# Optimization experiments

Measured on AMD Instinct MI355X. Metric: run time of the kernel, lower is better.

Reference implementation:

```python
import jax, jax.numpy as jnp
import numpy as np
import math

B, S, D, H, NC, K = 16, 512, 128, 8, 4, 7
DK = D // H
LN_EPS = 1e-5


def setup_inputs() -> dict:
    key = jax.random.key(0)
    ks = jax.random.split(key, 12)
    rn = lambda i, shape, scale: jax.random.normal(ks[i], shape, jnp.float32) * scale
    return {
        "x": rn(0, (B, S, D), 1.0),
        "mask": jnp.ones((B, S), jnp.int32),
        "ln_scale": jnp.ones((NC + 2, D), jnp.float32),
        "ln_bias": jnp.zeros((NC + 2, D), jnp.float32),
        "dw_w": rn(1, (NC, D, 1, K), 0.15),   # depthwise conv weights (OIH per layer)
        "dw_b": jnp.zeros((NC, D), jnp.float32),
        "pw_w": rn(2, (NC, D, D, 1), 0.08),   # pointwise conv weights
        "pw_b": jnp.zeros((NC, D), jnp.float32),
        "Wq": rn(3, (H, D, DK), 0.1),
        "Wk": rn(4, (H, D, DK), 0.1),
        "Wv": rn(5, (H, D, DK), 0.1),
        "Wo": rn(6, (D, D), 0.08),
        "att_bias": jnp.zeros((1,), jnp.float32),
        "f1_w": rn(7, (D, D), 0.08),
        "f1_b": jnp.zeros((D,), jnp.float32),
        "f2_w": rn(8, (D, D), 0.08),
        "f2_b": jnp.zeros((D,), jnp.float32),
        "l": 1,
        "blks": 7,
    }


def _ln(x, g, b):
    mu = jnp.mean(x, axis=-1, keepdims=True)
    var = jnp.mean((x - mu) ** 2, axis=-1, keepdims=True)
    return (x - mu) / jnp.sqrt(var + LN_EPS) * g + b


def _pos_signal(length, channels):
    position = jnp.arange(length, dtype=jnp.float32)
    nt = channels // 2
    inc = math.log(10000.0) / float(nt - 1)
    inv = jnp.exp(jnp.arange(nt, dtype=jnp.float32) * -inc)
    st = position[:, None] * inv[None, :]              # [L, nt]
    return jnp.concatenate([jnp.sin(st), jnp.cos(st)], axis=1)[None]  # [1, L, C]


def _encoder_block(x, mask, ln_scale, ln_bias, dw_w, dw_b, pw_w, pw_b,
                   Wq, Wk, Wv, Wo, att_bias, f1_w, f1_b, f2_w, f2_b):
    Bb, Ss, Dd = x.shape
    n_conv = dw_w.shape[0]
    k_size = dw_w.shape[-1]
    pad = k_size // 2
    dn = ('NCH', 'OIH', 'NCH')

    out = x + _pos_signal(Ss, Dd)
    # depthwise-separable conv stack (eval mode: dropout = identity)
    for i in range(n_conv):
        res = out
        h = _ln(out, ln_scale[i], ln_bias[i])
        hc = jnp.transpose(h, (0, 2, 1))  # [B, D, S]
        y = jax.lax.conv_general_dilated(hc, dw_w[i], (1,), [(pad, pad)],
                                         dimension_numbers=dn,
                                         feature_group_count=Dd)
        y = y + dw_b[i][None, :, None]
        y = jax.lax.conv_general_dilated(y, pw_w[i], (1,), [(0, 0)],
                                         dimension_numbers=dn)
        y = jax.nn.relu(y + pw_b[i][None, :, None])
        out = jnp.transpose(y, (0, 2, 1)) + res

    # multi-head self-attention (batched over heads, same math as per-head loop)
    res = out
    h = _ln(out, ln_scale[-2], ln_bias[-2])
    b0 = att_bias[0]
    q = jnp.einsum('bsd,hdk->bhsk', h, Wq) + b0
    k = jnp.einsum('bsd,hdk->bhsk', h, Wk) + b0
    v = jnp.einsum('bsd,hdk->bhsk', h, Wv) + b0
    scores = jnp.einsum('bhsk,bhtk->bhst', q, k) * (1.0 / math.sqrt(q.shape[-1]))
    m = mask.astype(scores.dtype)[:, None, None, :]  # mask over key axis
    scores = m * scores + (1.0 - m) * (-1e30)
    p = jax.nn.softmax(scores, axis=-1)
    att = jnp.einsum('bhst,bhtk->bhsk', p, v)          # [B,H,S,dk]
    mh = jnp.transpose(att, (0, 2, 1, 3)).reshape(Bb, Ss, Dd)
    out = mh @ Wo + b0 + res

    # feed-forward
    res = out
    h = _ln(out, ln_scale[-1], ln_bias[-1])
    h = jax.nn.relu(h @ f1_w.T + f1_b) @ f2_w.T + f2_b
    return h + res


def reference(x, mask, ln_scale, ln_bias, dw_w, dw_b, pw_w, pw_b,
              Wq, Wk, Wv, Wo, att_bias, f1_w, f1_b, f2_w, f2_b, l, blks):
    # l, blks only affect stochastic layer-dropout during training; eval = residual add
    return _encoder_block(x, mask, ln_scale, ln_bias, dw_w, dw_b, pw_w, pw_b,
                          Wq, Wk, Wv, Wo, att_bias, f1_w, f1_b, f2_w, f2_b)
```

## Files before the change

kernel.cpp:

```cpp
#include <hip/hip_runtime.h>
#include <math.h>

#define BB 16
#define SS 512
#define DD 128
#define HH 8
#define NCONV 4
#define KW 7
#define DKK 16
#define NN (BB*SS)
#define LN_EPS 1e-5f

typedef __attribute__((ext_vector_type(8))) short short8;
typedef __attribute__((ext_vector_type(4))) short short4v;
typedef __attribute__((ext_vector_type(4))) float f4;

static __device__ __forceinline__ ushort f2bf(float x) {
  union { float f; unsigned u; } v; v.f = x;
  unsigned r = v.u + 0x7fffu + ((v.u >> 16) & 1u);
  return (ushort)(r >> 16);
}

static __device__ __forceinline__ float posenc(int s, int col) {
  const float inc = 0.14619588f;
  int c = col & 63;
  float invf = expf(-inc * (float)c);
  float st = (float)s * invf;
  return (col < 64) ? sinf(st) : cosf(st);
}

__global__ __launch_bounds__(256) void prep_kernel(
    const float* __restrict__ pw, const float* __restrict__ Wq,
    const float* __restrict__ Wk, const float* __restrict__ Wv,
    const float* __restrict__ Wo, const float* __restrict__ f1,
    const float* __restrict__ f2, ushort* __restrict__ dst) {
  int i = blockIdx.x * 256 + threadIdx.x;
  if (i < 65536) { dst[i] = f2bf(pw[i]); return; }
  int j = i - 65536;
  if (j < 49152) {
    int o = j >> 7, d = j & 127;
    int sec = o >> 7, oo = o & 127, hh = oo >> 4, kk = oo & 15;
    const float* s = (sec == 0) ? Wq : ((sec == 1) ? Wk : Wv);
    dst[i] = f2bf(s[hh*2048 + d*16 + kk]); return;
  }
  j -= 49152;
  if (j < 16384) { int o = j >> 7, d = j & 127; dst[i] = f2bf(Wo[d*128 + o]); return; }
  j -= 16384;
  if (j < 16384) { dst[i] = f2bf(f1[j]); return; }
  j -= 16384;
  dst[i] = f2bf(f2[j]);
}

template<int LNORM, int ACT, int BIASMODE, int RES, int OUTBF>
__global__ __launch_bounds__(256) void mm16_kernel(
    const float* __restrict__ in_f, const ushort* __restrict__ in_b,
    const ushort* __restrict__ Wb,
    const float* __restrict__ gamma, const float* __restrict__ beta,
    const float* __restrict__ bias, const float* __restrict__ res,
    float* __restrict__ out_f, ushort* __restrict__ out_b, int ostride) {
  __shared__ ushort abuf[16*152];
  __shared__ ushort wbuf[128*152];
  int t = threadIdx.x;
  int r0 = blockIdx.x * 16;
  int ocol0 = blockIdx.y * 128;
  const ushort* W = Wb + blockIdx.y * (128*128);

  for (int i = t; i < 128*16; i += 256) {
    int row = i >> 4, ch = i & 15;
    *(short8*)&wbuf[row*152 + ch*8] = *(const short8*)&W[row*128 + ch*8];
  }
  int wv = t >> 6, lane = t & 63;
  if (LNORM) {
    for (int i = wv; i < 16; i += 4) {
      int r = r0 + i;
      float2 xv = *(const float2*)&in_f[r*128 + lane*2];
      float s1 = xv.x + xv.y, s2 = xv.x*xv.x + xv.y*xv.y;
      #pragma unroll
      for (int o = 32; o > 0; o >>= 1) { s1 += __shfl_xor(s1, o); s2 += __shfl_xor(s2, o); }
      float mu = s1 * (1.0f/128.0f);
      float var = s2 * (1.0f/128.0f) - mu*mu;
      float inv = rsqrtf(var + LN_EPS);
      float2 gv = *(const float2*)&gamma[lane*2];
      float2 bv = *(const float2*)&beta[lane*2];
      float n0 = (xv.x - mu)*inv*gv.x + bv.x;
      float n1 = (xv.y - mu)*inv*gv.y + bv.y;
      unsigned pk = (unsigned)f2bf(n0) | ((unsigned)f2bf(n1) << 16);
      *(unsigned*)&abuf[i*152 + lane*2] = pk;
    }
  } else {
    for (int i = t; i < 16*16; i += 256) {
      int row = i >> 4, ch = i & 15;
      *(short8*)&abuf[row*152 + ch*8] = *(const short8*)&in_b[(r0+row)*128 + ch*8];
    }
  }
  __syncthreads();

  int m = lane & 15, qd = lane >> 4;
  int c0 = wv * 32;
  f4 acc0 = {0.f,0.f,0.f,0.f}, acc1 = {0.f,0.f,0.f,0.f};
  #pragma unroll
  for (int ks = 0; ks < 4; ++ks) {
    short8 a  = *(const short8*)&abuf[m*152 + ks*32 + qd*8];
    short8 b0 = *(const short8*)&wbuf[(c0 + m)*152 + ks*32 + qd*8];
    short8 b1 = *(const short8*)&wbuf[(c0 + 16 + m)*152 + ks*32 + qd*8];
    acc0 = __builtin_amdgcn_mfma_f32_16x16x32_bf16(a, b0, acc0, 0, 0, 0);
    acc1 = __builtin_amdgcn_mfma_f32_16x16x32_bf16(a, b1, acc1, 0, 0, 0);
  }
  int col0 = c0 + m, col1 = c0 + 16 + m;
  float bv0 = (BIASMODE==1) ? bias[col0] : ((BIASMODE==2) ? bias[0] : 0.0f);
  float bv1 = (BIASMODE==1) ? bias[col1] : ((BIASMODE==2) ? bias[0] : 0.0f);
  #pragma unroll
  for (int reg = 0; reg < 4; ++reg) {
    int r = r0 + qd*4 + reg;
    float v0 = acc0[reg] + bv0, v1 = acc1[reg] + bv1;
    if (ACT) { v0 = fmaxf(v0, 0.0f); v1 = fmaxf(v1, 0.0f); }
    if (RES) { v0 += res[r*128 + col0]; v1 += res[r*128 + col1]; }
    if (OUTBF) {
      out_b[r*ostride + ocol0 + col0] = f2bf(v0);
      out_b[r*ostride + ocol0 + col1] = f2bf(v1);
    } else {
      out_f[r*ostride + ocol0 + col0] = v0;
      out_f[r*ostride + ocol0 + col1] = v1;
    }
  }
}

template<int ADDPOS>
__global__ __launch_bounds__(256) void conv_fused_kernel(
    const float* __restrict__ cur, const ushort* __restrict__ pwW,
    const float* __restrict__ gamma, const float* __restrict__ beta,
    const float* __restrict__ dww, const float* __restrict__ dwb,
    const float* __restrict__ pwb, float* __restrict__ out) {
  __shared__ float  hbuf[22*128];
  __shared__ ushort ybuf[16*152];
  __shared__ ushort wbuf[128*152];
  int t = threadIdx.x;
  int r0 = blockIdx.x * 16;
  int s0 = r0 & (SS-1);
  int bb = r0 >> 9;

  for (int i = t; i < 128*16; i += 256) {
    int row = i >> 4, ch = i & 15;
    *(short8*)&wbuf[row*152 + ch*8] = *(const short8*)&pwW[row*128 + ch*8];
  }
  int wv = t >> 6, lane = t & 63;
  for (int i = wv; i < 22; i += 4) {
    int s = s0 - 3 + i;
    if (s < 0 || s >= SS) {
      *(float2*)&hbuf[i*128 + lane*2] = make_float2(0.f, 0.f);
      continue;
    }
    int r = bb*SS + s;
    float2 xv = *(const float2*)&cur[r*128 + lane*2];
    if (ADDPOS) { xv.x += posenc(s, lane*2); xv.y += posenc(s, lane*2+1); }
    float s1 = xv.x + xv.y, s2 = xv.x*xv.x + xv.y*xv.y;
    #pragma unroll
    for (int o = 32; o > 0; o >>= 1) { s1 += __shfl_xor(s1, o); s2 += __shfl_xor(s2, o); }
    float mu = s1 * (1.0f/128.0f);
    float var = s2 * (1.0f/128.0f) - mu*mu;
    float inv = rsqrtf(var + LN_EPS);
    float2 gv = *(const float2*)&gamma[lane*2];
    float2 bv = *(const float2*)&beta[lane*2];
    hbuf[i*128 + lane*2]     = (xv.x - mu)*inv*gv.x + bv.x;
    hbuf[i*128 + lane*2 + 1] = (xv.y - mu)*inv*gv.y + bv.y;
  }
  __syncthreads();

  {
    int col = t & 127, rg = t >> 7;
    float w0 = dww[col*7+0], w1 = dww[col*7+1], w2 = dww[col*7+2], w3 = dww[col*7+3];
    float w4 = dww[col*7+4], w5 = dww[col*7+5], w6 = dww[col*7+6];
    float bs = dwb[col];
    #pragma unroll
    for (int rr = rg*8; rr < rg*8 + 8; ++rr) {
      float acc = bs;
      acc += hbuf[(rr+0)*128 + col] * w0;
      acc += hbuf[(rr+1)*128 + col] * w1;
      acc += hbuf[(rr+2)*128 + col] * w2;
      acc += hbuf[(rr+3)*128 + col] * w3;
      acc += hbuf[(rr+4)*128 + col] * w4;
      acc += hbuf[(rr+5)*128 + col] * w5;
      acc += hbuf[(rr+6)*128 + col] * w6;
      ybuf[rr*152 + col] = f2bf(acc);
    }
  }
  __syncthreads();

  int m = lane & 15, qd = lane >> 4;
  int c0 = wv * 32;
  f4 acc0 = {0.f,0.f,0.f,0.f}, acc1 = {0.f,0.f,0.f,0.f};
  #pragma unroll
  for (int ks = 0; ks < 4; ++ks) {
    short8 a  = *(const short8*)&ybuf[m*152 + ks*32 + qd*8];
    short8 b0 = *(const short8*)&wbuf[(c0 + m)*152 + ks*32 + qd*8];
    short8 b1 = *(const short8*)&wbuf[(c0 + 16 + m)*152 + ks*32 + qd*8];
    acc0 = __builtin_amdgcn_mfma_f32_16x16x32_bf16(a, b0, acc0, 0, 0, 0);
    acc1 = __builtin_amdgcn_mfma_f32_16x16x32_bf16(a, b1, acc1, 0, 0, 0);
  }
  int col0 = c0 + m, col1 = c0 + 16 + m;
  float bv0 = pwb[col0], bv1 = pwb[col1];
  #pragma unroll
  for (int reg = 0; reg < 4; ++reg) {
    int r = r0 + qd*4 + reg;
    int s = s0 + qd*4 + reg;
    float v0 = fmaxf(acc0[reg] + bv0, 0.0f);
    float v1 = fmaxf(acc1[reg] + bv1, 0.0f);
    float rz0 = cur[r*128 + col0], rz1 = cur[r*128 + col1];
    if (ADDPOS) { rz0 += posenc(s, col0); rz1 += posenc(s, col1); }
    out[r*128 + col0] = v0 + rz0;
    out[r*128 + col1] = v1 + rz1;
  }
}

__global__ __launch_bounds__(256) void attn_mfma_kernel(
    const ushort* __restrict__ qkv, const int* __restrict__ mask,
    ushort* __restrict__ att) {
  __shared__ ushort kbuf[512*24];
  __shared__ ushort vbuf[512*20];
  __shared__ ushort pbuf[4*16*40];
  __shared__ float  smask[512];
  int t = threadIdx.x;
  int blk = blockIdx.x;
  int qc = blk & 7, h = (blk >> 3) & 7, b = blk >> 6;

  for (int i = t; i < 512; i += 256) smask[i] = (float)mask[b*SS + i];
  for (int i = t; i < 1024; i += 256) {
    int s = i >> 1, half = i & 1;
    *(short8*)&kbuf[s*24 + half*8] =
      *(const short8*)&qkv[(size_t)(b*SS + s)*384 + 128 + h*16 + half*8];
  }
  for (int i = t; i < 2048; i += 256) {
    int s = i >> 2, qu = i & 3;
    *(short4v*)&vbuf[s*20 + qu*4] =
      *(const short4v*)&qkv[(size_t)(b*SS + s)*384 + 256 + h*16 + qu*4];
  }
  __syncthreads();

  int wv = t >> 6, lane = t & 63;
  int m = lane & 15, qd = lane >> 4;
  int qr0 = qc*64 + wv*16;

  short8 aq = (short8)0;
  if (qd < 2) aq = *(const short8*)&qkv[(size_t)(b*SS + qr0 + m)*384 + h*16 + qd*8];

  f4 oacc = {0.f,0.f,0.f,0.f};
  float lp0 = 0.f, lp1 = 0.f, lp2 = 0.f, lp3 = 0.f;
  ushort* pb = &pbuf[wv*640];
  f4 zz = {0.f,0.f,0.f,0.f};

  for (int step = 0; step < 16; ++step) {
    int kb = step * 32;
    short8 bk0 = (short8)0, bk1 = (short8)0;
    if (qd < 2) {
      bk0 = *(const short8*)&kbuf[(kb + m)*24 + qd*8];
      bk1 = *(const short8*)&kbuf[(kb + 16 + m)*24 + qd*8];
    }
    f4 s0 = __builtin_amdgcn_mfma_f32_16x16x32_bf16(aq, bk0, zz, 0, 0, 0);
    f4 s1 = __builtin_amdgcn_mfma_f32_16x16x32_bf16(aq, bk1, zz, 0, 0, 0);
    float mk0 = smask[kb + m], mk1 = smask[kb + 16 + m];
    #pragma unroll
    for (int reg = 0; reg < 4; ++reg) {
      float e0 = __expf(s0[reg] * 0.25f) * mk0;
      float e1 = __expf(s1[reg] * 0.25f) * mk1;
      if (reg == 0) { lp0 += e0 + e1; } else if (reg == 1) { lp1 += e0 + e1; }
      else if (reg == 2) { lp2 += e0 + e1; } else { lp3 += e0 + e1; }
      pb[(qd*4 + reg)*40 + m]      = f2bf(e0);
      pb[(qd*4 + reg)*40 + 16 + m] = f2bf(e1);
    }
    __asm__ volatile("s_waitcnt lgkmcnt(0)" ::: "memory");
    short8 ap = *(const short8*)&pb[m*40 + qd*8];
    short8 bv;
    #pragma unroll
    for (int j = 0; j < 8; ++j) bv[j] = (short)vbuf[(kb + qd*8 + j)*20 + m];
    oacc = __builtin_amdgcn_mfma_f32_16x16x32_bf16(ap, bv, oacc, 0, 0, 0);
  }

  float lp[4] = {lp0, lp1, lp2, lp3};
  #pragma unroll
  for (int reg = 0; reg < 4; ++reg) {
    float l = lp[reg];
    l += __shfl_xor(l, 1); l += __shfl_xor(l, 2);
    l += __shfl_xor(l, 4); l += __shfl_xor(l, 8);
    float ov = oacc[reg] / l;
    att[(size_t)(b*SS + qr0 + qd*4 + reg)*128 + h*16 + m] = f2bf(ov);
  }
}

extern "C" void kernel_launch(void* const* d_in, const int* in_sizes, int n_in,
                              void* d_out, int out_size, void* d_ws, size_t ws_size,
                              hipStream_t stream) {
  const float* x        = (const float*)d_in[0];
  const int*   mask     = (const int*)d_in[1];
  const float* ln_scale = (const float*)d_in[2];
  const float* ln_bias  = (const float*)d_in[3];
  const float* dw_w     = (const float*)d_in[4];
  const float* dw_b     = (const float*)d_in[5];
  const float* pw_w     = (const float*)d_in[6];
  const float* pw_b     = (const float*)d_in[7];
  const float* Wq       = (const float*)d_in[8];
  const float* Wk       = (const float*)d_in[9];
  const float* Wv       = (const float*)d_in[10];
  const float* Wo       = (const float*)d_in[11];
  const float* att_bias = (const float*)d_in[12];
  const float* f1_w     = (const float*)d_in[13];
  const float* f1_b     = (const float*)d_in[14];
  const float* f2_w     = (const float*)d_in[15];
  const float* f2_b     = (const float*)d_in[16];
  float* out = (float*)d_out;

  ushort* wall    = (ushort*)d_ws;
  ushort* pw_bf   = wall;
  ushort* wqkv_bf = wall + 65536;
  ushort* wo_bf   = wall + 114688;
  ushort* f1_bf   = wall + 131072;
  ushort* f2_bf   = wall + 147456;
  ushort* qkvbuf  = wall + 163840;
  ushort* attbuf  = qkvbuf + (size_t)NN*384;
  ushort* ybuf    = attbuf + (size_t)NN*128;

  hipLaunchKernelGGL(prep_kernel, dim3(640), dim3(256), 0, stream,
                     pw_w, Wq, Wk, Wv, Wo, f1_w, f2_w, wall);

  hipLaunchKernelGGL((conv_fused_kernel<1>), dim3(NN/16), dim3(256), 0, stream,
                     x, pw_bf, ln_scale, ln_bias, dw_w, dw_b, pw_b, out);
  for (int i = 1; i < NCONV; ++i) {
    hipLaunchKernelGGL((conv_fused_kernel<0>), dim3(NN/16), dim3(256), 0, stream,
                       out, pw_bf + i*16384, ln_scale + i*128, ln_bias + i*128,
                       dw_w + i*896, dw_b + i*128, pw_b + i*128, out);
  }

  hipLaunchKernelGGL((mm16_kernel<1,0,2,0,1>), dim3(NN/16, 3), dim3(256), 0, stream,
                     out, nullptr, wqkv_bf, ln_scale + 4*128, ln_bias + 4*128,
                     att_bias, nullptr, nullptr, qkvbuf, 384);

  hipLaunchKernelGGL(attn_mfma_kernel, dim3(BB*HH*8), dim3(256), 0, stream,
                     qkvbuf, mask, attbuf);

  hipLaunchKernelGGL((mm16_kernel<0,0,2,1,0>), dim3(NN/16, 1), dim3(256), 0, stream,
                     nullptr, attbuf, wo_bf, nullptr, nullptr,
                     att_bias, out, out, nullptr, 128);

  hipLaunchKernelGGL((mm16_kernel<1,1,1,0,1>), dim3(NN/16, 1), dim3(256), 0, stream,
                     out, nullptr, f1_bf, ln_scale + 5*128, ln_bias + 5*128,
                     f1_b, nullptr, nullptr, ybuf, 128);
  hipLaunchKernelGGL((mm16_kernel<0,0,1,1,0>), dim3(NN/16, 1), dim3(256), 0, stream,
                     nullptr, ybuf, f2_bf, nullptr, nullptr,
                     f2_b, out, out, nullptr, 128);
}
```

Before: 176.2 us.

## Fuse all stages into one cooperative persistent kernel with grid syncs

Replaces the ten separate kernel launches (weight prep, four conv layers, QKV, attention, Wo, FFN1, FFN2) with a single cooperative kernel of 512 blocks that runs each stage in turn, separated by grid.sync(). The tail fuses the Wo projection, layernorm, and both FFN matmuls per 16-row tile in shared memory. The conv layers ping-pong between two buffers, the depthwise conv is vectorised to float2, and V is stored transposed for the attention matmul. This removes launch gaps and intermediate global round-trips, at the cost of grid-barrier overhead and a fixed 512-block grid that may limit occupancy per stage.

```diff
diff --git a/kernel.cpp b/kernel.cpp
--- a/kernel.cpp
+++ b/kernel.cpp
@@ -1,13 +1,13 @@
 #include <hip/hip_runtime.h>
+#include <hip/hip_cooperative_groups.h>
 #include <math.h>
+
+namespace cg = cooperative_groups;
 
 #define BB 16
 #define SS 512
 #define DD 128
 #define HH 8
-#define NCONV 4
-#define KW 7
-#define DKK 16
 #define NN (BB*SS)
 #define LN_EPS 1e-5f
 
@@ -29,75 +29,15 @@
   return (col < 64) ? sinf(st) : cosf(st);
 }
 
-__global__ __launch_bounds__(256) void prep_kernel(
-    const float* __restrict__ pw, const float* __restrict__ Wq,
-    const float* __restrict__ Wk, const float* __restrict__ Wv,
-    const float* __restrict__ Wo, const float* __restrict__ f1,
-    const float* __restrict__ f2, ushort* __restrict__ dst) {
-  int i = blockIdx.x * 256 + threadIdx.x;
-  if (i < 65536) { dst[i] = f2bf(pw[i]); return; }
-  int j = i - 65536;
-  if (j < 49152) {
-    int o = j >> 7, d = j & 127;
-    int sec = o >> 7, oo = o & 127, hh = oo >> 4, kk = oo & 15;
-    const float* s = (sec == 0) ? Wq : ((sec == 1) ? Wk : Wv);
-    dst[i] = f2bf(s[hh*2048 + d*16 + kk]); return;
-  }
-  j -= 49152;
-  if (j < 16384) { int o = j >> 7, d = j & 127; dst[i] = f2bf(Wo[d*128 + o]); return; }
-  j -= 16384;
-  if (j < 16384) { dst[i] = f2bf(f1[j]); return; }
-  j -= 16384;
-  dst[i] = f2bf(f2[j]);
-}
-
-template<int LNORM, int ACT, int BIASMODE, int RES, int OUTBF>
-__global__ __launch_bounds__(256) void mm16_kernel(
-    const float* __restrict__ in_f, const ushort* __restrict__ in_b,
-    const ushort* __restrict__ Wb,
-    const float* __restrict__ gamma, const float* __restrict__ beta,
-    const float* __restrict__ bias, const float* __restrict__ res,
-    float* __restrict__ out_f, ushort* __restrict__ out_b, int ostride) {
-  __shared__ ushort abuf[16*152];
-  __shared__ ushort wbuf[128*152];
-  int t = threadIdx.x;
-  int r0 = blockIdx.x * 16;
-  int ocol0 = blockIdx.y * 128;
-  const ushort* W = Wb + blockIdx.y * (128*128);
-
-  for (int i = t; i < 128*16; i += 256) {
+static __device__ __forceinline__ void stage_w(ushort* wbuf, const ushort* W, int t) {
+  for (int i = t; i < 2048; i += 256) {
     int row = i >> 4, ch = i & 15;
     *(short8*)&wbuf[row*152 + ch*8] = *(const short8*)&W[row*128 + ch*8];
   }
-  int wv = t >> 6, lane = t & 63;
-  if (LNORM) {
-    for (int i = wv; i < 16; i += 4) {
-      int r = r0 + i;
-      float2 xv = *(const float2*)&in_f[r*128 + lane*2];
-      float s1 = xv.x + xv.y, s2 = xv.x*xv.x + xv.y*xv.y;
-      #pragma unroll
-      for (int o = 32; o > 0; o >>= 1) { s1 += __shfl_xor(s1, o); s2 += __shfl_xor(s2, o); }
-      float mu = s1 * (1.0f/128.0f);
-      float var = s2 * (1.0f/128.0f) - mu*mu;
-      float inv = rsqrtf(var + LN_EPS);
-      float2 gv = *(const float2*)&gamma[lane*2];
-      float2 bv = *(const float2*)&beta[lane*2];
-      float n0 = (xv.x - mu)*inv*gv.x + bv.x;
-      float n1 = (xv.y - mu)*inv*gv.y + bv.y;
-      unsigned pk = (unsigned)f2bf(n0) | ((unsigned)f2bf(n1) << 16);
-      *(unsigned*)&abuf[i*152 + lane*2] = pk;
-    }
-  } else {
-    for (int i = t; i < 16*16; i += 256) {
-      int row = i >> 4, ch = i & 15;
-      *(short8*)&abuf[row*152 + ch*8] = *(const short8*)&in_b[(r0+row)*128 + ch*8];
-    }
-  }
-  __syncthreads();
-
-  int m = lane & 15, qd = lane >> 4;
-  int c0 = wv * 32;
-  f4 acc0 = {0.f,0.f,0.f,0.f}, acc1 = {0.f,0.f,0.f,0.f};
+}
+
+static __device__ __forceinline__ void mm_tile(const ushort* abuf, const ushort* wbuf,
+                                               int m, int qd, int c0, f4& acc0, f4& acc1) {
   #pragma unroll
   for (int ks = 0; ks < 4; ++ks) {
     short8 a  = *(const short8*)&abuf[m*152 + ks*32 + qd*8];
@@ -106,43 +46,50 @@
     acc0 = __builtin_amdgcn_mfma_f32_16x16x32_bf16(a, b0, acc0, 0, 0, 0);
     acc1 = __builtin_amdgcn_mfma_f32_16x16x32_bf16(a, b1, acc1, 0, 0, 0);
   }
-  int col0 = c0 + m, col1 = c0 + 16 + m;
-  float bv0 = (BIASMODE==1) ? bias[col0] : ((BIASMODE==2) ? bias[0] : 0.0f);
-  float bv1 = (BIASMODE==1) ? bias[col1] : ((BIASMODE==2) ? bias[0] : 0.0f);
-  #pragma unroll
-  for (int reg = 0; reg < 4; ++reg) {
-    int r = r0 + qd*4 + reg;
-    float v0 = acc0[reg] + bv0, v1 = acc1[reg] + bv1;
-    if (ACT) { v0 = fmaxf(v0, 0.0f); v1 = fmaxf(v1, 0.0f); }
-    if (RES) { v0 += res[r*128 + col0]; v1 += res[r*128 + col1]; }
-    if (OUTBF) {
-      out_b[r*ostride + ocol0 + col0] = f2bf(v0);
-      out_b[r*ostride + ocol0 + col1] = f2bf(v1);
-    } else {
-      out_f[r*ostride + ocol0 + col0] = v0;
-      out_f[r*ostride + ocol0 + col1] = v1;
-    }
-  }
-}
-
-template<int ADDPOS>
-__global__ __launch_bounds__(256) void conv_fused_kernel(
-    const float* __restrict__ cur, const ushort* __restrict__ pwW,
-    const float* __restrict__ gamma, const float* __restrict__ beta,
-    const float* __restrict__ dww, const float* __restrict__ dwb,
-    const float* __restrict__ pwb, float* __restrict__ out) {
-  __shared__ float  hbuf[22*128];
-  __shared__ ushort ybuf[16*152];
-  __shared__ ushort wbuf[128*152];
+}
+
+static __device__ __forceinline__ void ln_rows_to_abuf(const float* in, int r0,
+    const float* gamma, const float* beta, ushort* abuf, int wv, int lane) {
+  for (int i = wv; i < 16; i += 4) {
+    float2 xv = *(const float2*)&in[(size_t)(r0 + i)*128 + lane*2];
+    float s1 = xv.x + xv.y, s2 = xv.x*xv.x + xv.y*xv.y;
+    #pragma unroll
+    for (int o = 32; o > 0; o >>= 1) { s1 += __shfl_xor(s1, o); s2 += __shfl_xor(s2, o); }
+    float mu  = s1 * (1.0f/128.0f);
+    float var = s2 * (1.0f/128.0f) - mu*mu;
+    float inv = rsqrtf(var + LN_EPS);
+    float2 gv = *(const float2*)&gamma[lane*2];
+    float2 bv = *(const float2*)&beta[lane*2];
+    float n0 = (xv.x - mu)*inv*gv.x + bv.x;
+    float n1 = (xv.y - mu)*inv*gv.y + bv.y;
+    unsigned pk = (unsigned)f2bf(n0) | ((unsigned)f2bf(n1) << 16);
+    *(unsigned*)&abuf[i*152 + lane*2] = pk;
+  }
+}
+
+struct MegaParams {
+  const float* x; const int* mask;
+  const float* ln_scale; const float* ln_bias;
+  const float* dw_w; const float* dw_b; const float* pw_w; const float* pw_b;
+  const float* Wq; const float* Wk; const float* Wv; const float* Wo;
+  const float* att_bias; const float* f1_w; const float* f1_b;
+  const float* f2_w; const float* f2_b;
+  float* out;
+  ushort* wbf; float* bufA; float* bufB; ushort* qkvbuf; ushort* attbuf;
+};
+
+static __device__ void conv_stage(unsigned char* smem, const float* in,
+    const ushort* pwW, const float* gamma, const float* beta,
+    const float* dww, const float* dwb, const float* pwb,
+    float* outp, bool addpos) {
+  float*  hbuf = (float*)smem;
+  ushort* wbuf = (ushort*)(smem + 11264);
+  ushort* ybuf = (ushort*)(smem + 50176);
   int t = threadIdx.x;
   int r0 = blockIdx.x * 16;
   int s0 = r0 & (SS-1);
   int bb = r0 >> 9;
-
-  for (int i = t; i < 128*16; i += 256) {
-    int row = i >> 4, ch = i & 15;
-    *(short8*)&wbuf[row*152 + ch*8] = *(const short8*)&pwW[row*128 + ch*8];
-  }
+  stage_w(wbuf, pwW, t);
   int wv = t >> 6, lane = t & 63;
   for (int i = wv; i < 22; i += 4) {
     int s = s0 - 3 + i;
@@ -151,12 +98,12 @@
       continue;
     }
     int r = bb*SS + s;
-    float2 xv = *(const float2*)&cur[r*128 + lane*2];
-    if (ADDPOS) { xv.x += posenc(s, lane*2); xv.y += posenc(s, lane*2+1); }
+    float2 xv = *(const float2*)&in[(size_t)r*128 + lane*2];
+    if (addpos) { xv.x += posenc(s, lane*2); xv.y += posenc(s, lane*2+1); }
     float s1 = xv.x + xv.y, s2 = xv.x*xv.x + xv.y*xv.y;
     #pragma unroll
     for (int o = 32; o > 0; o >>= 1) { s1 += __shfl_xor(s1, o); s2 += __shfl_xor(s2, o); }
-    float mu = s1 * (1.0f/128.0f);
+    float mu  = s1 * (1.0f/128.0f);
     float var = s2 * (1.0f/128.0f) - mu*mu;
     float inv = rsqrtf(var + LN_EPS);
     float2 gv = *(const float2*)&gamma[lane*2];
@@ -165,38 +112,30 @@
     hbuf[i*128 + lane*2 + 1] = (xv.y - mu)*inv*gv.y + bv.y;
   }
   __syncthreads();
-
   {
-    int col = t & 127, rg = t >> 7;
-    float w0 = dww[col*7+0], w1 = dww[col*7+1], w2 = dww[col*7+2], w3 = dww[col*7+3];
-    float w4 = dww[col*7+4], w5 = dww[col*7+5], w6 = dww[col*7+6];
-    float bs = dwb[col];
-    #pragma unroll
-    for (int rr = rg*8; rr < rg*8 + 8; ++rr) {
-      float acc = bs;
-      acc += hbuf[(rr+0)*128 + col] * w0;
-      acc += hbuf[(rr+1)*128 + col] * w1;
-      acc += hbuf[(rr+2)*128 + col] * w2;
-      acc += hbuf[(rr+3)*128 + col] * w3;
-      acc += hbuf[(rr+4)*128 + col] * w4;
-      acc += hbuf[(rr+5)*128 + col] * w5;
-      acc += hbuf[(rr+6)*128 + col] * w6;
-      ybuf[rr*152 + col] = f2bf(acc);
-    }
-  }
-  __syncthreads();
-
-  int m = lane & 15, qd = lane >> 4;
-  int c0 = wv * 32;
+    int cp = t & 63, rg = t >> 6;
+    float wa[7], wb2[7];
+    #pragma unroll
+    for (int k = 0; k < 7; ++k) { wa[k] = dww[(cp*2)*7 + k]; wb2[k] = dww[(cp*2+1)*7 + k]; }
+    float ba = dwb[cp*2], bbx = dwb[cp*2+1];
+    #pragma unroll
+    for (int j = 0; j < 4; ++j) {
+      int rr = rg*4 + j;
+      float a0 = ba, a1 = bbx;
+      #pragma unroll
+      for (int k = 0; k < 7; ++k) {
+        float2 hv = *(const float2*)&hbuf[(rr + k)*128 + cp*2];
+        a0 += hv.x * wa[k];
+        a1 += hv.y * wb2[k];
+      }
+      unsigned pk = (unsigned)f2bf(a0) | ((unsigned)f2bf(a1) << 16);
+      *(unsigned*)&ybuf[rr*152 + cp*2] = pk;
+    }
+  }
+  __syncthreads();
+  int m = lane & 15, qd = lane >> 4, c0 = wv*32;
   f4 acc0 = {0.f,0.f,0.f,0.f}, acc1 = {0.f,0.f,0.f,0.f};
-  #pragma unroll
-  for (int ks = 0; ks < 4; ++ks) {
-    short8 a  = *(const short8*)&ybuf[m*152 + ks*32 + qd*8];
-    short8 b0 = *(const short8*)&wbuf[(c0 + m)*152 + ks*32 + qd*8];
-    short8 b1 = *(const short8*)&wbuf[(c0 + 16 + m)*152 + ks*32 + qd*8];
-    acc0 = __builtin_amdgcn_mfma_f32_16x16x32_bf16(a, b0, acc0, 0, 0, 0);
-    acc1 = __builtin_amdgcn_mfma_f32_16x16x32_bf16(a, b1, acc1, 0, 0, 0);
-  }
+  mm_tile(ybuf, wbuf, m, qd, c0, acc0, acc1);
   int col0 = c0 + m, col1 = c0 + 16 + m;
   float bv0 = pwb[col0], bv1 = pwb[col1];
   #pragma unroll
@@ -205,25 +144,47 @@
     int s = s0 + qd*4 + reg;
     float v0 = fmaxf(acc0[reg] + bv0, 0.0f);
     float v1 = fmaxf(acc1[reg] + bv1, 0.0f);
-    float rz0 = cur[r*128 + col0], rz1 = cur[r*128 + col1];
-    if (ADDPOS) { rz0 += posenc(s, col0); rz1 += posenc(s, col1); }
-    out[r*128 + col0] = v0 + rz0;
-    out[r*128 + col1] = v1 + rz1;
-  }
-}
-
-__global__ __launch_bounds__(256) void attn_mfma_kernel(
-    const ushort* __restrict__ qkv, const int* __restrict__ mask,
-    ushort* __restrict__ att) {
-  __shared__ ushort kbuf[512*24];
-  __shared__ ushort vbuf[512*20];
-  __shared__ ushort pbuf[4*16*40];
-  __shared__ float  smask[512];
-  int t = threadIdx.x;
-  int blk = blockIdx.x;
-  int qc = blk & 7, h = (blk >> 3) & 7, b = blk >> 6;
-
-  for (int i = t; i < 512; i += 256) smask[i] = (float)mask[b*SS + i];
+    float rz0 = in[(size_t)r*128 + col0], rz1 = in[(size_t)r*128 + col1];
+    if (addpos) { rz0 += posenc(s, col0); rz1 += posenc(s, col1); }
+    outp[(size_t)r*128 + col0] = v0 + rz0;
+    outp[(size_t)r*128 + col1] = v1 + rz1;
+  }
+}
+
+static __device__ void qkv_stage(unsigned char* smem, const float* in,
+    const ushort* wqkv, const float* gamma, const float* beta,
+    float b0, ushort* qkvout) {
+  ushort* abuf = (ushort*)smem;
+  ushort* wbuf = (ushort*)(smem + 4864);
+  int t = threadIdx.x, wv = t >> 6, lane = t & 63;
+  int r0 = blockIdx.x * 16;
+  ln_rows_to_abuf(in, r0, gamma, beta, abuf, wv, lane);
+  int m = lane & 15, qd = lane >> 4, c0 = wv*32;
+  for (int c = 0; c < 3; ++c) {
+    __syncthreads();
+    stage_w(wbuf, wqkv + c*16384, t);
+    __syncthreads();
+    f4 acc0 = {0.f,0.f,0.f,0.f}, acc1 = {0.f,0.f,0.f,0.f};
+    mm_tile(abuf, wbuf, m, qd, c0, acc0, acc1);
+    int col0 = c0 + m, col1 = c0 + 16 + m;
+    #pragma unroll
+    for (int reg = 0; reg < 4; ++reg) {
+      int r = r0 + qd*4 + reg;
+      qkvout[(size_t)r*384 + c*128 + col0] = f2bf(acc0[reg] + b0);
+      qkvout[(size_t)r*384 + c*128 + col1] = f2bf(acc1[reg] + b0);
+    }
+  }
+}
+
+static __device__ void attn_stage(unsigned char* smem, const ushort* qkv,
+    const int* maskp, ushort* att) {
+  ushort* kbuf  = (ushort*)smem;
+  ushort* vT    = (ushort*)(smem + 24576);
+  ushort* pbuf  = (ushort*)(smem + 41216);
+  float*  smask = (float*)(smem + 46336);
+  int t = threadIdx.x, blk = blockIdx.x;
+  int qc = blk & 3, h = (blk >> 2) & 7, b = blk >> 5;
+  for (int i = t; i < 512; i += 256) smask[i] = (float)maskp[b*SS + i];
   for (int i = t; i < 1024; i += 256) {
     int s = i >> 1, half = i & 1;
     *(short8*)&kbuf[s*24 + half*8] =
@@ -231,119 +192,191 @@
   }
   for (int i = t; i < 2048; i += 256) {
     int s = i >> 2, qu = i & 3;
-    *(short4v*)&vbuf[s*20 + qu*4] =
-      *(const short4v*)&qkv[(size_t)(b*SS + s)*384 + 256 + h*16 + qu*4];
-  }
-  __syncthreads();
-
-  int wv = t >> 6, lane = t & 63;
-  int m = lane & 15, qd = lane >> 4;
-  int qr0 = qc*64 + wv*16;
-
-  short8 aq = (short8)0;
-  if (qd < 2) aq = *(const short8*)&qkv[(size_t)(b*SS + qr0 + m)*384 + h*16 + qd*8];
-
-  f4 oacc = {0.f,0.f,0.f,0.f};
-  float lp0 = 0.f, lp1 = 0.f, lp2 = 0.f, lp3 = 0.f;
+    short4v v = *(const short4v*)&qkv[(size_t)(b*SS + s)*384 + 256 + h*16 + qu*4];
+    #pragma unroll
+    for (int j = 0; j < 4; ++j) vT[(qu*4 + j)*520 + s] = (ushort)v[j];
+  }
+  __syncthreads();
+  int wv = t >> 6, lane = t & 63, m = lane & 15, qd = lane >> 4;
   ushort* pb = &pbuf[wv*640];
   f4 zz = {0.f,0.f,0.f,0.f};
-
-  for (int step = 0; step < 16; ++step) {
-    int kb = step * 32;
-    short8 bk0 = (short8)0, bk1 = (short8)0;
-    if (qd < 2) {
-      bk0 = *(const short8*)&kbuf[(kb + m)*24 + qd*8];
-      bk1 = *(const short8*)&kbuf[(kb + 16 + m)*24 + qd*8];
-    }
-    f4 s0 = __builtin_amdgcn_mfma_f32_16x16x32_bf16(aq, bk0, zz, 0, 0, 0);
-    f4 s1 = __builtin_amdgcn_mfma_f32_16x16x32_bf16(aq, bk1, zz, 0, 0, 0);
-    float mk0 = smask[kb + m], mk1 = smask[kb + 16 + m];
-    #pragma unroll
-    for (int reg = 0; reg < 4; ++reg) {
-      float e0 = __expf(s0[reg] * 0.25f) * mk0;
-      float e1 = __expf(s1[reg] * 0.25f) * mk1;
-      if (reg == 0) { lp0 += e0 + e1; } else if (reg == 1) { lp1 += e0 + e1; }
-      else if (reg == 2) { lp2 += e0 + e1; } else { lp3 += e0 + e1; }
-      pb[(qd*4 + reg)*40 + m]      = f2bf(e0);
-      pb[(qd*4 + reg)*40 + 16 + m] = f2bf(e1);
-    }
-    __asm__ volatile("s_waitcnt lgkmcnt(0)" ::: "memory");
-    short8 ap = *(const short8*)&pb[m*40 + qd*8];
-    short8 bv;
-    #pragma unroll
-    for (int j = 0; j < 8; ++j) bv[j] = (short)vbuf[(kb + qd*8 + j)*20 + m];
-    oacc = __builtin_amdgcn_mfma_f32_16x16x32_bf16(ap, bv, oacc, 0, 0, 0);
-  }
-
-  float lp[4] = {lp0, lp1, lp2, lp3};
-  #pragma unroll
-  for (int reg = 0; reg < 4; ++reg) {
-    float l = lp[reg];
-    l += __shfl_xor(l, 1); l += __shfl_xor(l, 2);
-    l += __shfl_xor(l, 4); l += __shfl_xor(l, 8);
-    float ov = oacc[reg] / l;
-    att[(size_t)(b*SS + qr0 + qd*4 + reg)*128 + h*16 + m] = f2bf(ov);
-  }
+  for (int sub = 0; sub < 2; ++sub) {
+    int qr0 = qc*128 + sub*64 + wv*16;
+    short8 aq = (short8)0;
+    if (qd < 2) aq = *(const short8*)&qkv[(size_t)(b*SS + qr0 + m)*384 + h*16 + qd*8];
+    f4 oacc = zz;
+    float lp0 = 0.f, lp1 = 0.f, lp2 = 0.f, lp3 = 0.f;
+    for (int step = 0; step < 16; ++step) {
+      int kb = step * 32;
+      short8 bk0 = (short8)0, bk1 = (short8)0;
+      if (qd < 2) {
+        bk0 = *(const short8*)&kbuf[(kb + m)*24 + qd*8];
+        bk1 = *(const short8*)&kbuf[(kb + 16 + m)*24 + qd*8];
+      }
+      f4 s0 = __builtin_amdgcn_mfma_f32_16x16x32_bf16(aq, bk0, zz, 0, 0, 0);
+      f4 s1 = __builtin_amdgcn_mfma_f32_16x16x32_bf16(aq, bk1, zz, 0, 0, 0);
+      float mk0 = smask[kb + m], mk1 = smask[kb + 16 + m];
+      #pragma unroll
+      for (int reg = 0; reg < 4; ++reg) {
+        float e0 = __expf(s0[reg] * 0.25f) * mk0;
+        float e1 = __expf(s1[reg] * 0.25f) * mk1;
+        if (reg == 0) lp0 += e0 + e1; else if (reg == 1) lp1 += e0 + e1;
+        else if (reg == 2) lp2 += e0 + e1; else lp3 += e0 + e1;
+        pb[(qd*4 + reg)*40 + m]      = f2bf(e0);
+        pb[(qd*4 + reg)*40 + 16 + m] = f2bf(e1);
+      }
+      __asm__ volatile("s_waitcnt lgkmcnt(0)" ::: "memory");
+      short8 ap = *(const short8*)&pb[m*40 + qd*8];
+      short8 bv = *(const short8*)&vT[m*520 + kb + qd*8];
+      oacc = __builtin_amdgcn_mfma_f32_16x16x32_bf16(ap, bv, oacc, 0, 0, 0);
+    }
+    float lp[4] = {lp0, lp1, lp2, lp3};
+    #pragma unroll
+    for (int reg = 0; reg < 4; ++reg) {
+      float l = lp[reg];
+      l += __shfl_xor(l, 1); l += __shfl_xor(l, 2);
+      l += __shfl_xor(l, 4); l += __shfl_xor(l, 8);
+      att[(size_t)(b*SS + qr0 + qd*4 + reg)*128 + h*16 + m] = f2bf(oacc[reg] / l);
+    }
+  }
+}
+
+static __device__ void tail_stage(unsigned char* smem, const ushort* attb,
+    const float* resA, const ushort* wo, const ushort* f1w, const ushort* f2w,
+    const float* gamma, const float* beta, float b0,
+    const float* f1_bias, const float* f2_bias, float* outp) {
+  float*  hres = (float*)smem;
+  ushort* wbuf = (ushort*)(smem + 8192);
+  ushort* abuf = (ushort*)(smem + 47104);
+  ushort* ybuf = (ushort*)(smem + 51968);
+  int t = threadIdx.x, wv = t >> 6, lane = t & 63;
+  int m = lane & 15, qd = lane >> 4, c0 = wv*32;
+  int r0 = blockIdx.x * 16;
+  stage_w(wbuf, wo, t);
+  for (int i = t; i < 256; i += 256) {
+    int row = i >> 4, ch = i & 15;
+    *(short8*)&abuf[row*152 + ch*8] = *(const short8*)&attb[(size_t)(r0 + row)*128 + ch*8];
+  }
+  __syncthreads();
+  {
+    f4 acc0 = {0.f,0.f,0.f,0.f}, acc1 = {0.f,0.f,0.f,0.f};
+    mm_tile(abuf, wbuf, m, qd, c0, acc0, acc1);
+    int col0 = c0 + m, col1 = c0 + 16 + m;
+    #pragma unroll
+    for (int reg = 0; reg < 4; ++reg) {
+      int lr = qd*4 + reg, r = r0 + lr;
+      hres[lr*128 + col0] = acc0[reg] + b0 + resA[(size_t)r*128 + col0];
+      hres[lr*128 + col1] = acc1[reg] + b0 + resA[(size_t)r*128 + col1];
+    }
+  }
+  __syncthreads();
+  ln_rows_to_abuf(hres, 0, gamma, beta, abuf, wv, lane);
+  stage_w(wbuf, f1w, t);
+  __syncthreads();
+  {
+    f4 acc0 = {0.f,0.f,0.f,0.f}, acc1 = {0.f,0.f,0.f,0.f};
+    mm_tile(abuf, wbuf, m, qd, c0, acc0, acc1);
+    int col0 = c0 + m, col1 = c0 + 16 + m;
+    float bv0 = f1_bias[col0], bv1 = f1_bias[col1];
+    #pragma unroll
+    for (int reg = 0; reg < 4; ++reg) {
+      int lr = qd*4 + reg;
+      ybuf[lr*152 + col0] = f2bf(fmaxf(acc0[reg] + bv0, 0.0f));
+      ybuf[lr*152 + col1] = f2bf(fmaxf(acc1[reg] + bv1, 0.0f));
+    }
+  }
+  __syncthreads();
+  stage_w(wbuf, f2w, t);
+  __syncthreads();
+  {
+    f4 acc0 = {0.f,0.f,0.f,0.f}, acc1 = {0.f,0.f,0.f,0.f};
+    mm_tile(ybuf, wbuf, m, qd, c0, acc0, acc1);
+    int col0 = c0 + m, col1 = c0 + 16 + m;
+    float bv0 = f2_bias[col0], bv1 = f2_bias[col1];
+    #pragma unroll
+    for (int reg = 0; reg < 4; ++reg) {
+      int lr = qd*4 + reg, r = r0 + lr;
+      outp[(size_t)r*128 + col0] = acc0[reg] + bv0 + hres[lr*128 + col0];
+      outp[(size_t)r*128 + col1] = acc1[reg] + bv1 + hres[lr*128 + col1];
+    }
+  }
+}
+
+__global__ __launch_bounds__(256, 2) void mega_kernel(MegaParams p) {
+  __shared__ __align__(16) unsigned char smem[57344];
+  cg::grid_group grid = cg::this_grid();
+  int t = threadIdx.x;
+
+  for (int i = blockIdx.x*256 + t; i < 163840; i += 131072) {
+    ushort val;
+    if (i < 65536) { val = f2bf(p.pw_w[i]); }
+    else {
+      int j = i - 65536;
+      if (j < 49152) {
+        int o = j >> 7, d = j & 127;
+        int sec = o >> 7, oo = o & 127, hh = oo >> 4, kk = oo & 15;
+        const float* s = (sec == 0) ? p.Wq : ((sec == 1) ? p.Wk : p.Wv);
+        val = f2bf(s[hh*2048 + d*16 + kk]);
+      } else {
+        j -= 49152;
+        if (j < 16384) { int o = j >> 7, d = j & 127; val = f2bf(p.Wo[d*128 + o]); }
+        else { j -= 16384;
+          if (j < 16384) val = f2bf(p.f1_w[j]);
+          else val = f2bf(p.f2_w[j - 16384]);
+        }
+      }
+    }
+    p.wbf[i] = val;
+  }
+  grid.sync();
+
+  conv_stage(smem, p.x,    p.wbf,         p.ln_scale,     p.ln_bias,     p.dw_w,       p.dw_b,       p.pw_b,       p.bufB, true);
+  grid.sync();
+  conv_stage(smem, p.bufB, p.wbf+16384, p.ln_scale+128, p.ln_bias+128, p.dw_w+896,  p.dw_b+128,  p.pw_b+128,  p.bufA, false);
+  grid.sync();
+  conv_stage(smem, p.bufA, p.wbf+32768, p.ln_scale+256, p.ln_bias+256, p.dw_w+1792, p.dw_b+256,  p.pw_b+256,  p.bufB, false);
+  grid.sync();
+  conv_stage(smem, p.bufB, p.wbf+49152, p.ln_scale+384, p.ln_bias+384, p.dw_w+2688, p.dw_b+384,  p.pw_b+384,  p.bufA, false);
+  grid.sync();
+
+  float b0 = p.att_bias[0];
+  qkv_stage(smem, p.bufA, p.wbf+65536, p.ln_scale+512, p.ln_bias+512, b0, p.qkvbuf);
+  grid.sync();
+  attn_stage(smem, p.qkvbuf, p.mask, p.attbuf);
+  grid.sync();
+  tail_stage(smem, p.attbuf, p.bufA, p.wbf+114688, p.wbf+131072, p.wbf+147456,
+             p.ln_scale+640, p.ln_bias+640, b0, p.f1_b, p.f2_b, p.out);
 }
 
 extern "C" void kernel_launch(void* const* d_in, const int* in_sizes, int n_in,
                               void* d_out, int out_size, void* d_ws, size_t ws_size,
                               hipStream_t stream) {
-  const float* x        = (const float*)d_in[0];
-  const int*   mask     = (const int*)d_in[1];
-  const float* ln_scale = (const float*)d_in[2];
-  const float* ln_bias  = (const float*)d_in[3];
-  const float* dw_w     = (const float*)d_in[4];
-  const float* dw_b     = (const float*)d_in[5];
-  const float* pw_w     = (const float*)d_in[6];
-  const float* pw_b     = (const float*)d_in[7];
-  const float* Wq       = (const float*)d_in[8];
-  const float* Wk       = (const float*)d_in[9];
-  const float* Wv       = (const float*)d_in[10];
-  const float* Wo       = (const float*)d_in[11];
-  const float* att_bias = (const float*)d_in[12];
-  const float* f1_w     = (const float*)d_in[13];
-  const float* f1_b     = (const float*)d_in[14];
-  const float* f2_w     = (const float*)d_in[15];
-  const float* f2_b     = (const float*)d_in[16];
-  float* out = (float*)d_out;
-
-  ushort* wall    = (ushort*)d_ws;
-  ushort* pw_bf   = wall;
-  ushort* wqkv_bf = wall + 65536;
-  ushort* wo_bf   = wall + 114688;
-  ushort* f1_bf   = wall + 131072;
-  ushort* f2_bf   = wall + 147456;
-  ushort* qkvbuf  = wall + 163840;
-  ushort* attbuf  = qkvbuf + (size_t)NN*384;
-  ushort* ybuf    = attbuf + (size_t)NN*128;
-
-  hipLaunchKernelGGL(prep_kernel, dim3(640), dim3(256), 0, stream,
-                     pw_w, Wq, Wk, Wv, Wo, f1_w, f2_w, wall);
-
-  hipLaunchKernelGGL((conv_fused_kernel<1>), dim3(NN/16), dim3(256), 0, stream,
-                     x, pw_bf, ln_scale, ln_bias, dw_w, dw_b, pw_b, out);
-  for (int i = 1; i < NCONV; ++i) {
-    hipLaunchKernelGGL((conv_fused_kernel<0>), dim3(NN/16), dim3(256), 0, stream,
-                       out, pw_bf + i*16384, ln_scale + i*128, ln_bias + i*128,
-                       dw_w + i*896, dw_b + i*128, pw_b + i*128, out);
-  }
-
-  hipLaunchKernelGGL((mm16_kernel<1,0,2,0,1>), dim3(NN/16, 3), dim3(256), 0, stream,
-                     out, nullptr, wqkv_bf, ln_scale + 4*128, ln_bias + 4*128,
-                     att_bias, nullptr, nullptr, qkvbuf, 384);
-
-  hipLaunchKernelGGL(attn_mfma_kernel, dim3(BB*HH*8), dim3(256), 0, stream,
-                     qkvbuf, mask, attbuf);
-
-  hipLaunchKernelGGL((mm16_kernel<0,0,2,1,0>), dim3(NN/16, 1), dim3(256), 0, stream,
-                     nullptr, attbuf, wo_bf, nullptr, nullptr,
-                     att_bias, out, out, nullptr, 128);
-
-  hipLaunchKernelGGL((mm16_kernel<1,1,1,0,1>), dim3(NN/16, 1), dim3(256), 0, stream,
-                     out, nullptr, f1_bf, ln_scale + 5*128, ln_bias + 5*128,
-                     f1_b, nullptr, nullptr, ybuf, 128);
-  hipLaunchKernelGGL((mm16_kernel<0,0,1,1,0>), dim3(NN/16, 1), dim3(256), 0, stream,
-                     nullptr, ybuf, f2_bf, nullptr, nullptr,
-                     f2_b, out, out, nullptr, 128);
-}
+  MegaParams p;
+  p.x        = (const float*)d_in[0];
+  p.mask     = (const int*)d_in[1];
+  p.ln_scale = (const float*)d_in[2];
+  p.ln_bias  = (const float*)d_in[3];
+  p.dw_w     = (const float*)d_in[4];
+  p.dw_b     = (const float*)d_in[5];
+  p.pw_w     = (const float*)d_in[6];
+  p.pw_b     = (const float*)d_in[7];
+  p.Wq       = (const float*)d_in[8];
+  p.Wk       = (const float*)d_in[9];
+  p.Wv       = (const float*)d_in[10];
+  p.Wo       = (const float*)d_in[11];
+  p.att_bias = (const float*)d_in[12];
+  p.f1_w     = (const float*)d_in[13];
+  p.f1_b     = (const float*)d_in[14];
+  p.f2_w     = (const float*)d_in[15];
+  p.f2_b     = (const float*)d_in[16];
+  p.out      = (float*)d_out;
+
+  p.wbf    = (ushort*)d_ws;
+  p.bufA   = (float*)((char*)d_ws + 327680);
+  p.bufB   = p.bufA + (size_t)NN*128;
+  p.qkvbuf = (ushort*)(p.bufB + (size_t)NN*128);
+  p.attbuf = p.qkvbuf + (size_t)NN*384;
+
+  void* args[] = { &p };
+  hipLaunchCooperativeKernel((void*)mega_kernel, dim3(512), dim3(256), args, 0, stream);
+}
```

Measured after the change: 579.8 us. 229% more time.
